# Performance work log

Hardware: AMD Instinct MI355X
Metric: run time of the kernel (lower is better)

The kernel has to match this reference:

```python
import jax, jax.numpy as jnp
import numpy as np

B, T, D = 4096, 200, 64
H0, H1 = 128, 64
NEG = float(-2**32 + 1)  # tf padding value


def setup_inputs() -> dict:
    key = jax.random.key(0)
    ks = jax.random.split(key, 8)
    q = jax.random.normal(ks[0], (B, D), dtype=jnp.float32)
    k = jax.random.normal(ks[1], (B, T, D), dtype=jnp.float32)
    v = jax.random.normal(ks[2], (B, T, D), dtype=jnp.float32)
    mask = jax.random.randint(ks[3], (B, T), 0, 2).astype(jnp.int32)
    W0 = jax.random.normal(ks[4], (4 * D, H0), dtype=jnp.float32) * (1.0 / np.sqrt(4 * D))
    b0 = jnp.zeros((H0,), dtype=jnp.float32)
    W1 = jax.random.normal(ks[5], (H0, H1), dtype=jnp.float32) * (1.0 / np.sqrt(H0))
    b1 = jnp.zeros((H1,), dtype=jnp.float32)
    Wf = jax.random.normal(ks[6], (H1, 1), dtype=jnp.float32) * (1.0 / np.sqrt(H1))
    bf = jnp.zeros((1,), dtype=jnp.float32)
    return {"q": q, "k": k, "v": v, "mask": mask,
            "W0": W0, "b0": b0, "W1": W1, "b1": b1, "Wf": Wf, "bf": bf}


def reference(q, k, v, mask, W0, b0, W1, b1, Wf, bf):
    # tile q across history positions: [B, D] -> [B, T, D]
    qt = jnp.broadcast_to(q[:, None, :], k.shape)
    # DIN interaction features: [B, T, 4D]
    info = jnp.concatenate([qt, k, qt - k, qt * k], axis=-1)
    # small scorer MLP (Dense+relu, Dense+relu, Dense(1))
    h = jax.nn.relu(jnp.einsum('btf,fh->bth', info, W0) + b0)
    h = jax.nn.relu(jnp.einsum('btf,fh->bth', h, W1) + b1)
    logits = (jnp.einsum('btf,fh->bth', h, Wf) + bf)[..., 0]  # [B, T]
    # mask then softmax over history
    logits = jnp.where(mask == 0, NEG, logits)
    att = jax.nn.softmax(logits, axis=-1)  # [B, T]
    # weighted pooling: [B, T] x [B, T, D] -> [B, D]
    return jnp.einsum('bt,btd->bd', att, v)
```

## Files before the change

kernel.cpp:

```cpp
#include <hip/hip_runtime.h>

typedef __attribute__((ext_vector_type(4))) _Float16 f16x4;
typedef __attribute__((ext_vector_type(8))) _Float16 f16x8;
typedef __attribute__((ext_vector_type(4))) float f32x4;

#define NB 4096
#define TT 200
#define DD 64
#define H0 128
#define H1 64
#define BT 512

#define WS_BC 0
#define WS_DD 16384
#define WS_W1 32768
#define WS_CB 49152

__global__ __launch_bounds__(256)
void pre_fold(const float* __restrict__ W0, const float* __restrict__ W1,
              unsigned char* __restrict__ ws)
{
  int idx = blockIdx.x * 256 + threadIdx.x;
  _Float16* bcT  = (_Float16*)(ws + WS_BC);
  _Float16* ddT  = (_Float16*)(ws + WS_DD);
  _Float16* w1p  = (_Float16*)(ws + WS_W1);
  if (idx < 8192) {
    int h = idx >> 6, d = idx & 63;
    bcT[h * 64 + d] = (_Float16)(W0[(64 + d) * H0 + h] - W0[(128 + d) * H0 + h]);
    ddT[h * 64 + d] = (_Float16)(W0[(192 + d) * H0 + h]);
  } else {
    int i = idx - 8192;
    int jrow = i >> 7, p = i & 127;
    int m = p >> 5, g4p = (p >> 3) & 3, jj = p & 7;
    int h = 32 * m + 16 * (jj >> 2) + 4 * g4p + (jj & 3);
    int up = p >> 3, wi = p & 7;
    w1p[jrow * 128 + (((up ^ (jrow & 15)) << 3) | wi)] = (_Float16)W1[h * H1 + jrow];
  }
}

__global__ __launch_bounds__(256)
void pre_cb(const float* __restrict__ q, const float* __restrict__ W0,
            const float* __restrict__ b0, unsigned char* __restrict__ ws)
{
  __shared__ float WacS[DD * H0];
  __shared__ float qS2[2][DD];
  const int tid = threadIdx.x;
  float* cb = (float*)(ws + WS_CB);

  #pragma unroll 4
  for (int i = 0; i < 32; ++i) {
    int idx = i * 256 + tid;
    int d = idx >> 7, h = idx & 127;
    WacS[idx] = W0[d * H0 + h] + W0[(128 + d) * H0 + h];
  }
  __syncthreads();

  const int half = tid >> 7, h = tid & 127;
  #pragma unroll 1
  for (int p = 0; p < 16; ++p) {
    int bpair = blockIdx.x * 32 + p * 2;
    if (tid < DD) qS2[0][tid] = q[(size_t)bpair * DD + tid];
    else if (tid >= 128 && tid < 128 + DD) qS2[1][tid - 128] = q[(size_t)(bpair + 1) * DD + (tid - 128)];
    __syncthreads();
    float s = b0[h];
    #pragma unroll 8
    for (int d = 0; d < DD; ++d) s = fmaf(qS2[half][d], WacS[d * H0 + h], s);
    cb[(size_t)(bpair + half) * H0 + h] = s;
    __syncthreads();
  }
}

__global__ __launch_bounds__(BT, 4)
void din_attn(const float* __restrict__ q, const float* __restrict__ k,
              const float* __restrict__ v, const int* __restrict__ mask,
              const float* __restrict__ b1, const float* __restrict__ Wf,
              const unsigned char* __restrict__ ws, float* __restrict__ out)
{
  const int tid  = threadIdx.x;
  const int bloc = tid >> 8;
  const int t256 = tid & 255;
  const int lane = tid & 63;
  const int wid4 = (tid >> 6) & 3;
  const int r16  = lane & 15;
  const int g4   = lane >> 4;
  const int b    = blockIdx.x * 2 + bloc;

  __shared__ __align__(16) _Float16 W1p[H1 * 128];
  __shared__ __align__(16) _Float16 MhT2[2][H0 * 64];
  __shared__ __align__(16) float qS[2][DD];
  __shared__ __align__(16) float cbS[2][H0];
  __shared__ __align__(16) float b1S[H1];
  __shared__ __align__(16) float WfS[H1];
  __shared__ __align__(16) float owav[2][4][DD];
  __shared__ float msv[2][4];
  __shared__ float ssv[2][4];

  const float* qb = q + (size_t)b * DD;
  const float* kb = k + (size_t)b * TT * DD;
  const float* vb = v + (size_t)b * TT * DD;
  const int*   mb = mask + (size_t)b * TT;

  {
    const uint4* src = (const uint4*)(ws + WS_W1);
    uint4* dst = (uint4*)W1p;
    dst[tid]       = src[tid];
    dst[512 + tid] = src[512 + tid];
  }
  if (t256 < DD) qS[bloc][t256] = qb[t256];
  else if (t256 >= 64 && t256 < 64 + H0)
    cbS[bloc][t256 - 64] = ((const float*)(ws + WS_CB))[(size_t)b * H0 + (t256 - 64)];
  if (tid >= 192 && tid < 192 + H1) b1S[tid - 192] = b1[tid - 192];
  if (tid >= 448 && tid < 448 + H1) WfS[tid - 448] = Wf[tid - 448];
  __syncthreads();

  {
    const _Float16* bcT = (const _Float16*)(ws + WS_BC);
    const _Float16* ddT = (const _Float16*)(ws + WS_DD);
    _Float16* Mh = MhT2[bloc];
    const int u    = t256 & 7;
    const int dblk = u * 8;
    const int h4 = (t256 >> 3) * 4;
    float q8[8];
    #pragma unroll
    for (int j = 0; j < 8; ++j) q8[j] = qS[bloc][dblk + j];
    #pragma unroll
    for (int hi = 0; hi < 4; ++hi) {
      const int h = h4 + hi;
      f16x8 bc8 = *(const f16x8*)(bcT + h * 64 + dblk);
      f16x8 dd8 = *(const f16x8*)(ddT + h * 64 + dblk);
      f16x8 o8;
      #pragma unroll
      for (int j = 0; j < 8; ++j)
        o8[j] = (_Float16)((float)bc8[j] + q8[j] * (float)dd8[j]);
      *(f16x8*)(&Mh[h * 64 + ((u ^ (h & 7)) << 3)]) = o8;
    }
  }
  __syncthreads();

  const int dof = 8 * g4;
  const int k8 = r16 & 7;
  const int kW = r16;
  const int tg = lane >> 4;
  const int dq = lane & 15;
  const _Float16* Mh = MhT2[bloc];

  float m_run = -3e30f, s_run = 0.f;
  f32x4 o4 = {0.f, 0.f, 0.f, 0.f};

  #pragma unroll 1
  for (int s = wid4; s < 13; s += 4) {
    const int t0   = s * 16;
    const int trow = t0 + r16;
    int mm = (trow < TT) ? mb[trow] : -1;

    f16x8 bh0, bh1;
    {
      const float* kp = kb + (trow < TT ? trow : TT - 1) * DD;
      float4 kq0 = *(const float4*)(kp + dof);
      float4 kq1 = *(const float4*)(kp + dof + 4);
      float4 kq2 = *(const float4*)(kp + 32 + dof);
      float4 kq3 = *(const float4*)(kp + 32 + dof + 4);
      float f0[8] = {kq0.x, kq0.y, kq0.z, kq0.w, kq1.x, kq1.y, kq1.z, kq1.w};
      float f1[8] = {kq2.x, kq2.y, kq2.z, kq2.w, kq3.x, kq3.y, kq3.z, kq3.w};
      #pragma unroll
      for (int j = 0; j < 8; ++j) {
        bh0[j] = (_Float16)f0[j];
        bh1[j] = (_Float16)f1[j];
      }
    }
    f32x4 vv0, vv1, vv2, vv3;
    {
      int ta = t0 + 0 + tg,  tb2 = t0 + 4 + tg;
      int tc = t0 + 8 + tg,  td = t0 + 12 + tg;
      vv0 = *(const f32x4*)(vb + (ta  < TT ? ta  : TT - 1) * DD + dq * 4);
      vv1 = *(const f32x4*)(vb + (tb2 < TT ? tb2 : TT - 1) * DD + dq * 4);
      vv2 = *(const f32x4*)(vb + (tc  < TT ? tc  : TT - 1) * DD + dq * 4);
      vv3 = *(const f32x4*)(vb + (td  < TT ? td  : TT - 1) * DD + dq * 4);
    }

    f32x4 acc1[4];
    #pragma unroll
    for (int c1 = 0; c1 < 4; ++c1) acc1[c1] = (f32x4){0.f, 0.f, 0.f, 0.f};

    #pragma unroll 1
    for (int m = 0; m < 4; ++m) {
      const _Float16* rowE = &Mh[((2 * m) * 16 + r16) * 64];
      const _Float16* rowO = rowE + 16 * 64;
      f16x8 afE0 = *(const f16x8*)(rowE + ((g4 ^ k8) << 3));
      f16x8 afE1 = *(const f16x8*)(rowE + (((g4 + 4) ^ k8) << 3));
      f32x4 a0e = {0.f, 0.f, 0.f, 0.f};
      a0e = __builtin_amdgcn_mfma_f32_16x16x32_f16(afE0, bh0, a0e, 0, 0, 0);
      a0e = __builtin_amdgcn_mfma_f32_16x16x32_f16(afE1, bh1, a0e, 0, 0, 0);
      f16x8 afO0 = *(const f16x8*)(rowO + ((g4 ^ k8) << 3));
      f16x8 afO1 = *(const f16x8*)(rowO + (((g4 + 4) ^ k8) << 3));
      f32x4 a0o = {0.f, 0.f, 0.f, 0.f};
      a0o = __builtin_amdgcn_mfma_f32_16x16x32_f16(afO0, bh0, a0o, 0, 0, 0);
      a0o = __builtin_amdgcn_mfma_f32_16x16x32_f16(afO1, bh1, a0o, 0, 0, 0);

      f32x4 cbe = *(const f32x4*)(&cbS[bloc][(2 * m) * 16 + 4 * g4]);
      f32x4 cbo = *(const f32x4*)(&cbS[bloc][(2 * m) * 16 + 16 + 4 * g4]);
      f16x8 hf;
      #pragma unroll
      for (int r = 0; r < 4; ++r) {
        float he = a0e[r] + cbe[r];
        float ho = a0o[r] + cbo[r];
        hf[r]     = (_Float16)(he > 0.f ? he : 0.f);
        hf[4 + r] = (_Float16)(ho > 0.f ? ho : 0.f);
      }
      #pragma unroll
      for (int c1 = 0; c1 < 4; ++c1) {
        f16x8 af1 = *(const f16x8*)(&W1p[(c1 * 16 + r16) * 128
                                         + (((4 * m + g4) ^ kW) << 3)]);
        acc1[c1] = __builtin_amdgcn_mfma_f32_16x16x32_f16(af1, hf, acc1[c1], 0, 0, 0);
      }
    }

    float p = 0.f;
    #pragma unroll
    for (int c1 = 0; c1 < 4; ++c1) {
      f32x4 b14 = *(const f32x4*)(&b1S[c1 * 16 + 4 * g4]);
      f32x4 wf4 = *(const f32x4*)(&WfS[c1 * 16 + 4 * g4]);
      #pragma unroll
      for (int r = 0; r < 4; ++r) {
        float h1 = acc1[c1][r] + b14[r];
        h1 = h1 > 0.f ? h1 : 0.f;
        p = fmaf(h1, wf4[r], p);
      }
    }
    p += __shfl_xor(p, 16, 64);
    p += __shfl_xor(p, 32, 64);
    p = (mm == 1) ? p : (mm == 0 ? -1e30f : -2e30f);

    float sm = p;
    sm = fmaxf(sm, __shfl_xor(sm, 1, 64));
    sm = fmaxf(sm, __shfl_xor(sm, 2, 64));
    sm = fmaxf(sm, __shfl_xor(sm, 4, 64));
    sm = fmaxf(sm, __shfl_xor(sm, 8, 64));
    float m_new = fmaxf(m_run, sm);
    float scale = __expf(m_run - m_new);
    s_run *= scale;
    #pragma unroll
    for (int j = 0; j < 4; ++j) o4[j] *= scale;
    {
      float w0 = __expf(__shfl(p,  0 + tg, 64) - m_new);
      float w1 = __expf(__shfl(p,  4 + tg, 64) - m_new);
      float w2 = __expf(__shfl(p,  8 + tg, 64) - m_new);
      float w3 = __expf(__shfl(p, 12 + tg, 64) - m_new);
      s_run += (w0 + w1) + (w2 + w3);
      #pragma unroll
      for (int j = 0; j < 4; ++j)
        o4[j] = fmaf(w0, vv0[j], fmaf(w1, vv1[j], fmaf(w2, vv2[j], fmaf(w3, vv3[j], o4[j]))));
    }
    m_run = m_new;
  }

  #pragma unroll
  for (int j = 0; j < 4; ++j) {
    o4[j] += __shfl_xor(o4[j], 16, 64);
    o4[j] += __shfl_xor(o4[j], 32, 64);
  }
  s_run += __shfl_xor(s_run, 16, 64);
  s_run += __shfl_xor(s_run, 32, 64);
  if (lane < 16) {
    *(f32x4*)(&owav[bloc][wid4][lane * 4]) = o4;
    if (lane == 0) { msv[bloc][wid4] = m_run; ssv[bloc][wid4] = s_run; }
  }
  __syncthreads();

  if (t256 < DD) {
    float m0 = msv[bloc][0], m1 = msv[bloc][1];
    float m2 = msv[bloc][2], m3 = msv[bloc][3];
    float mstar = fmaxf(fmaxf(m0, m1), fmaxf(m2, m3));
    float f0 = __expf(m0 - mstar), f1 = __expf(m1 - mstar);
    float f2 = __expf(m2 - mstar), f3 = __expf(m3 - mstar);
    float acc = owav[bloc][0][t256] * f0 + owav[bloc][1][t256] * f1
              + owav[bloc][2][t256] * f2 + owav[bloc][3][t256] * f3;
    float stot = ssv[bloc][0] * f0 + ssv[bloc][1] * f1
               + ssv[bloc][2] * f2 + ssv[bloc][3] * f3;
    out[(size_t)b * DD + t256] = acc / stot;
  }
}

extern "C" void kernel_launch(void* const* d_in, const int* in_sizes, int n_in,
                              void* d_out, int out_size, void* d_ws, size_t ws_size,
                              hipStream_t stream) {
  const float* q    = (const float*)d_in[0];
  const float* k    = (const float*)d_in[1];
  const float* v    = (const float*)d_in[2];
  const int*   mask = (const int*)d_in[3];
  const float* W0   = (const float*)d_in[4];
  const float* b0   = (const float*)d_in[5];
  const float* W1   = (const float*)d_in[6];
  const float* b1   = (const float*)d_in[7];
  const float* Wf   = (const float*)d_in[8];
  float* out = (float*)d_out;
  unsigned char* ws = (unsigned char*)d_ws;

  pre_fold<<<dim3(64), dim3(256), 0, stream>>>(W0, W1, ws);
  pre_cb<<<dim3(128), dim3(256), 0, stream>>>(q, W0, b0, ws);
  din_attn<<<dim3(NB / 2), dim3(BT), 0, stream>>>(q, k, v, mask, b1, Wf, ws, out);
}
```

Before: 113.7 us.

## Raise occupancy to five blocks per CU by cutting registers and LDS

Raises the launch bound from 4 to 5 blocks per CU. To fit, the V rows are loaded late, one at a time right before their FMA, instead of all four being prefetched before the MFMA section. The final reduction buffers now reuse the MhT2 shared array behind an extra barrier, which shrinks LDS per block. This trades memory-latency hiding for V loads against more resident waves, and the tighter register cap may cause spills.

```diff
diff --git a/kernel.cpp b/kernel.cpp
--- a/kernel.cpp
+++ b/kernel.cpp
@@ -70,7 +70,7 @@
   }
 }
 
-__global__ __launch_bounds__(BT, 4)
+__global__ __launch_bounds__(BT, 5)
 void din_attn(const float* __restrict__ q, const float* __restrict__ k,
               const float* __restrict__ v, const int* __restrict__ mask,
               const float* __restrict__ b1, const float* __restrict__ Wf,
@@ -91,9 +91,6 @@
   __shared__ __align__(16) float cbS[2][H0];
   __shared__ __align__(16) float b1S[H1];
   __shared__ __align__(16) float WfS[H1];
-  __shared__ __align__(16) float owav[2][4][DD];
-  __shared__ float msv[2][4];
-  __shared__ float ssv[2][4];
 
   const float* qb = q + (size_t)b * DD;
   const float* kb = k + (size_t)b * TT * DD;
@@ -167,15 +164,6 @@
         bh0[j] = (_Float16)f0[j];
         bh1[j] = (_Float16)f1[j];
       }
-    }
-    f32x4 vv0, vv1, vv2, vv3;
-    {
-      int ta = t0 + 0 + tg,  tb2 = t0 + 4 + tg;
-      int tc = t0 + 8 + tg,  td = t0 + 12 + tg;
-      vv0 = *(const f32x4*)(vb + (ta  < TT ? ta  : TT - 1) * DD + dq * 4);
-      vv1 = *(const f32x4*)(vb + (tb2 < TT ? tb2 : TT - 1) * DD + dq * 4);
-      vv2 = *(const f32x4*)(vb + (tc  < TT ? tc  : TT - 1) * DD + dq * 4);
-      vv3 = *(const f32x4*)(vb + (td  < TT ? td  : TT - 1) * DD + dq * 4);
     }
 
     f32x4 acc1[4];
@@ -247,9 +235,20 @@
       float w2 = __expf(__shfl(p,  8 + tg, 64) - m_new);
       float w3 = __expf(__shfl(p, 12 + tg, 64) - m_new);
       s_run += (w0 + w1) + (w2 + w3);
-      #pragma unroll
-      for (int j = 0; j < 4; ++j)
-        o4[j] = fmaf(w0, vv0[j], fmaf(w1, vv1[j], fmaf(w2, vv2[j], fmaf(w3, vv3[j], o4[j]))));
+      const int ta = t0 + tg;
+      f32x4 v4;
+      v4 = *(const f32x4*)(vb + (ta      < TT ? ta      : TT - 1) * DD + dq * 4);
+      #pragma unroll
+      for (int j = 0; j < 4; ++j) o4[j] = fmaf(w0, v4[j], o4[j]);
+      v4 = *(const f32x4*)(vb + (ta + 4  < TT ? ta + 4  : TT - 1) * DD + dq * 4);
+      #pragma unroll
+      for (int j = 0; j < 4; ++j) o4[j] = fmaf(w1, v4[j], o4[j]);
+      v4 = *(const f32x4*)(vb + (ta + 8  < TT ? ta + 8  : TT - 1) * DD + dq * 4);
+      #pragma unroll
+      for (int j = 0; j < 4; ++j) o4[j] = fmaf(w2, v4[j], o4[j]);
+      v4 = *(const f32x4*)(vb + (ta + 12 < TT ? ta + 12 : TT - 1) * DD + dq * 4);
+      #pragma unroll
+      for (int j = 0; j < 4; ++j) o4[j] = fmaf(w3, v4[j], o4[j]);
     }
     m_run = m_new;
   }
@@ -261,22 +260,21 @@
   }
   s_run += __shfl_xor(s_run, 16, 64);
   s_run += __shfl_xor(s_run, 32, 64);
-  if (lane < 16) {
-    *(f32x4*)(&owav[bloc][wid4][lane * 4]) = o4;
-    if (lane == 0) { msv[bloc][wid4] = m_run; ssv[bloc][wid4] = s_run; }
-  }
+
+  __syncthreads();
+  float* ob = (float*)&MhT2[bloc][0];
+  if (lane < 16) *(f32x4*)(&ob[wid4 * 64 + lane * 4]) = o4;
+  if (lane == 0) { ob[256 + wid4] = m_run; ob[264 + wid4] = s_run; }
   __syncthreads();
 
   if (t256 < DD) {
-    float m0 = msv[bloc][0], m1 = msv[bloc][1];
-    float m2 = msv[bloc][2], m3 = msv[bloc][3];
+    float m0 = ob[256], m1 = ob[257], m2 = ob[258], m3 = ob[259];
     float mstar = fmaxf(fmaxf(m0, m1), fmaxf(m2, m3));
     float f0 = __expf(m0 - mstar), f1 = __expf(m1 - mstar);
     float f2 = __expf(m2 - mstar), f3 = __expf(m3 - mstar);
-    float acc = owav[bloc][0][t256] * f0 + owav[bloc][1][t256] * f1
-              + owav[bloc][2][t256] * f2 + owav[bloc][3][t256] * f3;
-    float stot = ssv[bloc][0] * f0 + ssv[bloc][1] * f1
-               + ssv[bloc][2] * f2 + ssv[bloc][3] * f3;
+    float acc = ob[t256] * f0 + ob[64 + t256] * f1
+              + ob[128 + t256] * f2 + ob[192 + t256] * f3;
+    float stot = ob[264] * f0 + ob[265] * f1 + ob[266] * f2 + ob[267] * f3;
     out[(size_t)b * DD + t256] = acc / stot;
   }
 }
```

Result: slower. 160.0 us (+40.8%).
